# Performance work log

Measured on AMD Instinct MI355X. Metric: run time of the kernel, lower is better.

Reference implementation:

```python
import jax, jax.numpy as jnp
import numpy as np

EPS = 1e-12  # F.normalize default eps
TEMPERATURE = 0.1


def setup_inputs() -> dict:
    key = jax.random.key(0)
    ks = jax.random.split(key, 7)
    B, C, H, W = 8, 640, 64, 64
    R, KD = 4, 160           # max_refs, key_dim = context_dim // compress_ratio
    hh, ww = H // 4, W // 4  # cached value resolution from adaptive_avg_pool2d
    return {
        "current_context": jax.random.normal(ks[0], (B, C, H, W), dtype=jnp.float32),
        "Wq": jax.random.normal(ks[1], (KD, C), dtype=jnp.float32) * 0.02,  # query_proj 1x1 conv weight
        "bq": jax.random.normal(ks[2], (KD,), dtype=jnp.float32) * 0.02,
        "memory_keys": jax.random.normal(ks[3], (R, KD), dtype=jnp.float32),
        "value_cache": jax.random.normal(ks[4], (R, B, C, hh, ww), dtype=jnp.float32),
        "Wg": jax.random.normal(ks[5], (C, 2 * C), dtype=jnp.float32) * 0.02,  # fusion_gate 1x1 conv weight
        "bg": jax.random.normal(ks[6], (C,), dtype=jnp.float32) * 0.02,
        "k": 2,
    }


def reference(current_context, Wq, bq, memory_keys, value_cache, Wg, bg, k):
    B, C, H, W = current_context.shape
    R, B2, C2, hh, ww = value_cache.shape

    # query_proj (1x1 conv) then global average pool == pool then linear
    xm = current_context.mean(axis=(2, 3))                    # [B, C]
    query = xm @ Wq.T + bq                                    # [B, KD]

    # cosine similarity between query and all (fully-initialized) memory keys
    qn = query / jnp.maximum(jnp.linalg.norm(query, axis=1, keepdims=True), EPS)
    kn = memory_keys / jnp.maximum(jnp.linalg.norm(memory_keys, axis=1, keepdims=True), EPS)
    sims = qn @ kn.T                                          # [B, R]

    topv, topi = jax.lax.top_k(sims, k)                       # [B, k]
    attn = jax.nn.softmax(topv / TEMPERATURE, axis=1)         # [B, k]

    # gather cached (pooled) values per (batch, top-k index)
    gathered = value_cache[topi, jnp.arange(B)[:, None]]      # [B, k, C, hh, ww]

    # bilinear upsample (half-pixel centers == torch align_corners=False)
    resized = jax.image.resize(gathered.reshape(B * k, C, hh, ww),
                               (B * k, C, H, W), method="linear")
    resized = resized.reshape(B, k, C, H, W)

    weighted_ref = jnp.einsum("bkchw,bk->bchw", resized, attn)  # [B, C, H, W]

    # fusion gate: sigmoid(Conv1x1(cat([x, weighted_ref], dim=1))) without materializing cat
    W1, W2 = Wg[:, :C], Wg[:, C:]
    gate_pre = (jnp.einsum("bdhw,cd->bchw", current_context, W1)
                + jnp.einsum("bdhw,cd->bchw", weighted_ref, W2)
                + bg[None, :, None, None])
    gate = jax.nn.sigmoid(gate_pre)

    fused = gate * weighted_ref + (1.0 - gate) * current_context
    return fused
```

## Files before the change

kernel.cpp:

```cpp
#include <hip/hip_runtime.h>
#include <hip/hip_bf16.h>
#include <stdint.h>

#define BB 8
#define CC 640
#define HWSZ 4096
#define RR 4
#define KD 160
#define VH 16
#define VW 16
#define KW 1280
#define KX 640
#define TEMP 0.1f

#define BM 128
#define BN 64
#define BK 64

typedef __bf16 bf16x8 __attribute__((ext_vector_type(8)));
typedef short  short8 __attribute__((ext_vector_type(8)));
typedef float  f32x4  __attribute__((ext_vector_type(4)));

__device__ __forceinline__ unsigned short f2bf(float f) {
    union { float f; uint32_t u; } v; v.f = f;
    uint32_t u = v.u;
    uint32_t r = u + 0x7FFFu + ((u >> 16) & 1u);
    return (unsigned short)(r >> 16);
}
__device__ __forceinline__ float bf2f(unsigned short s) {
    union { uint32_t u; float f; } v; v.u = ((uint32_t)s) << 16;
    return v.f;
}

__global__ void k_mean(const float* __restrict__ cc, float* __restrict__ xm) {
    int plane = blockIdx.x;
    const float4* p4 = (const float4*)(cc + (size_t)plane * HWSZ);
    int t = threadIdx.x;
    float s = 0.f;
    #pragma unroll
    for (int i = 0; i < 4; i++) {
        float4 v = p4[t + i * 256];
        s += v.x + v.y + v.z + v.w;
    }
    #pragma unroll
    for (int off = 32; off; off >>= 1) s += __shfl_down(s, off);
    __shared__ float red[4];
    if ((t & 63) == 0) red[t >> 6] = s;
    __syncthreads();
    if (t == 0) xm[plane] = (red[0] + red[1] + red[2] + red[3]) * (1.f / HWSZ);
}

__global__ void k_wbf(const float* __restrict__ Wg, unsigned short* __restrict__ Wbf) {
    int i = (blockIdx.x * 256 + threadIdx.x) * 8;
    short8 o;
    #pragma unroll
    for (int j = 0; j < 8; j++) o[j] = (short)f2bf(Wg[i + j]);
    *(short8*)&Wbf[i] = o;
}

__global__ void k_query(const float* __restrict__ xm, const float* __restrict__ Wq,
                        const float* __restrict__ bq, float* __restrict__ q) {
    int o = blockIdx.x;
    int b = o / KD, j = o % KD;
    int lane = threadIdx.x;
    const float* xr = xm + b * CC;
    const float* wr = Wq + (size_t)j * CC;
    float p = 0.f;
    #pragma unroll
    for (int i = 0; i < CC / 64; i++) {
        int kk = lane + i * 64;
        p += xr[kk] * wr[kk];
    }
    #pragma unroll
    for (int off = 32; off; off >>= 1) p += __shfl_down(p, off);
    if (lane == 0) q[o] = p + bq[j];
}

__global__ void k_attn2(const float* __restrict__ q, const float* __restrict__ mk,
                        float* __restrict__ attnw, int* __restrict__ topidx) {
    int t = threadIdx.x, lane = t & 63, b = t >> 6;
    __shared__ float smk[RR * KD];
    for (int i = t; i < RR * KD; i += 512) smk[i] = mk[i];
    __syncthreads();
    const float* qr = q + b * KD;
    float qv[3];
    float s = 0.f;
    #pragma unroll
    for (int i = 0; i < 3; i++) {
        int idx = lane + i * 64;
        qv[i] = (idx < KD) ? qr[idx] : 0.f;
        s += qv[i] * qv[i];
    }
    #pragma unroll
    for (int off = 32; off; off >>= 1) s += __shfl_xor(s, off);
    float qn = fmaxf(sqrtf(s), 1e-12f);
    float sims[RR];
    #pragma unroll
    for (int r = 0; r < RR; r++) {
        float d = 0.f, kn2 = 0.f;
        #pragma unroll
        for (int i = 0; i < 3; i++) {
            int idx = lane + i * 64;
            float m = (idx < KD) ? smk[r * KD + idx] : 0.f;
            d += qv[i] * m;
            kn2 += m * m;
        }
        #pragma unroll
        for (int off = 32; off; off >>= 1) {
            d += __shfl_xor(d, off);
            kn2 += __shfl_xor(kn2, off);
        }
        sims[r] = d / (qn * fmaxf(sqrtf(kn2), 1e-12f));
    }
    if (lane == 0) {
        int i1 = 0;
        for (int r = 1; r < RR; r++) if (sims[r] > sims[i1]) i1 = r;
        int i2 = -1;
        for (int r = 0; r < RR; r++) { if (r == i1) continue; if (i2 < 0 || sims[r] > sims[i2]) i2 = r; }
        float e2 = expf((sims[i2] - sims[i1]) / TEMP);
        float a1 = 1.f / (1.f + e2);
        attnw[b * 2 + 0] = a1;
        attnw[b * 2 + 1] = e2 * a1;
        topidx[b * 2 + 0] = i1;
        topidx[b * 2 + 1] = i2;
    }
}

__global__ void k_wref(const float* __restrict__ vc, const float* __restrict__ attnw,
                       const int* __restrict__ topidx, unsigned short* __restrict__ wrb,
                       unsigned short* __restrict__ combT) {
    int blk = blockIdx.x;
    int b = blk / CC, c = blk % CC;
    __shared__ float plane[VH * VW];
    int t = threadIdx.x;
    int i1 = topidx[b * 2], i2 = topidx[b * 2 + 1];
    float a1 = attnw[b * 2], a2 = attnw[b * 2 + 1];
    const float* p1 = vc + ((size_t)(i1 * BB + b) * CC + c) * (VH * VW);
    const float* p2 = vc + ((size_t)(i2 * BB + b) * CC + c) * (VH * VW);
    plane[t] = a1 * p1[t] + a2 * p2[t];
    __syncthreads();
    combT[((size_t)((b << 8) + t)) * KX + c] = f2bf(plane[t]);
    unsigned short* out = wrb + ((size_t)b * CC + c) * HWSZ;
    #pragma unroll
    for (int i = 0; i < 16; i++) {
        int idx = t + i * 256;
        int y = idx >> 6, x = idx & 63;
        float py = y * 0.25f - 0.375f;
        int iy = (int)floorf(py);
        float fy = py - (float)iy;
        int y0 = max(iy, 0), y1 = min(iy + 1, VH - 1);
        float px = x * 0.25f - 0.375f;
        int ix = (int)floorf(px);
        float fx = px - (float)ix;
        int x0 = max(ix, 0), x1 = min(ix + 1, VW - 1);
        float v00 = plane[y0 * VW + x0], v01 = plane[y0 * VW + x1];
        float v10 = plane[y1 * VW + x0], v11 = plane[y1 * VW + x1];
        float v = (1.f - fy) * ((1.f - fx) * v00 + fx * v01)
                +        fy  * ((1.f - fx) * v10 + fx * v11);
        out[idx] = f2bf(v);
    }
}

__global__ void k_xpose(const float* __restrict__ cc, unsigned short* __restrict__ Xbf) {
    int g = blockIdx.x * 256 + threadIdx.x;
    int p = g & (HWSZ - 1);
    int idx = g >> 12;
    int kc = idx % 80;
    int b = idx / 80;
    const float* s = cc + ((size_t)(b * CC + kc * 8)) * HWSZ + p;
    short8 o;
    #pragma unroll
    for (int j = 0; j < 8; j++) o[j] = (short)f2bf(s[(size_t)j * HWSZ]);
    *(short8*)&Xbf[((size_t)b * HWSZ + p) * KX + kc * 8] = o;
}

__global__ __launch_bounds__(256) void k_gemmlow(
    const unsigned short* __restrict__ Wbf,
    const unsigned short* __restrict__ combT,
    unsigned short* __restrict__ glow)
{
    __shared__ unsigned short Wt[BM * BK];
    __shared__ unsigned short Xt[BN * BK];

    const int t = threadIdx.x;
    const int lane = t & 63;
    const int w = t >> 6;
    const int mt = blockIdx.x;
    const int n0 = blockIdx.y * BN;
    const int b = n0 >> 8;
    const int yx0 = n0 & 255;
    const int mbase = mt * BM;

    f32x4 acc[4][2];
    #pragma unroll
    for (int i = 0; i < 4; i++)
        #pragma unroll
        for (int j = 0; j < 2; j++) acc[i][j] = (f32x4){0.f, 0.f, 0.f, 0.f};

    const int wm = (w >> 1) * 64;
    const int wn = (w & 1) * 32;
    const int lrow = lane & 15;
    const int lkoff = (lane >> 4) * 8;

    const int srow = t >> 3, spos = t & 7;
    const int soct = spos ^ (srow & 7);

    const unsigned short* wsrc0 = Wbf + (size_t)mbase * KW + CC;
    const unsigned short* xsrc0 = combT + (size_t)n0 * KX;
    const int ldsbase = (t & ~63) * 8;

    for (int ks = 0; ks < KX / BK; ks++) {
        const int kb = ks * BK;
        if (ks) __syncthreads();
        #pragma unroll
        for (int i = 0; i < 4; i++) {
            const unsigned short* gw = wsrc0 + (size_t)(i * 32 + srow) * KW + kb + soct * 8;
            unsigned short* lw = &Wt[i * 2048 + ldsbase];
            __builtin_amdgcn_global_load_lds((const __attribute__((address_space(1))) void*)gw,
                                             (__attribute__((address_space(3))) void*)lw, 16, 0, 0);
        }
        #pragma unroll
        for (int i = 0; i < 2; i++) {
            const unsigned short* gx = xsrc0 + (size_t)(i * 32 + srow) * KX + kb + soct * 8;
            unsigned short* lx = &Xt[i * 2048 + ldsbase];
            __builtin_amdgcn_global_load_lds((const __attribute__((address_space(1))) void*)gx,
                                             (__attribute__((address_space(3))) void*)lx, 16, 0, 0);
        }
        __syncthreads();

        #pragma unroll
        for (int ki = 0; ki < 2; ki++) {
            bf16x8 af[4], bfr[2];
            const int kk = ki * 32 + lkoff;
            #pragma unroll
            for (int mi = 0; mi < 4; mi++) {
                int row = wm + mi * 16 + lrow;
                af[mi] = *(const bf16x8*)&Wt[row * BK + (kk ^ ((row & 7) << 3))];
            }
            #pragma unroll
            for (int ni = 0; ni < 2; ni++) {
                int prow = wn + ni * 16 + lrow;
                bfr[ni] = *(const bf16x8*)&Xt[prow * BK + (kk ^ ((prow & 7) << 3))];
            }
            #pragma unroll
            for (int mi = 0; mi < 4; mi++)
                #pragma unroll
                for (int ni = 0; ni < 2; ni++)
                    acc[mi][ni] = __builtin_amdgcn_mfma_f32_16x16x32_bf16(af[mi], bfr[ni], acc[mi][ni], 0, 0, 0);
        }
    }

    #pragma unroll
    for (int mi = 0; mi < 4; mi++) {
        #pragma unroll
        for (int r = 0; r < 4; r++) {
            int ch = mbase + wm + mi * 16 + (lane >> 4) * 4 + r;
            #pragma unroll
            for (int ni = 0; ni < 2; ni++) {
                int yx = yx0 + wn + ni * 16 + (lane & 15);
                glow[(((size_t)b * CC + ch) << 8) + yx] = f2bf(acc[mi][ni][r]);
            }
        }
    }
}

__global__ __launch_bounds__(256) void k_gemm(
    const unsigned short* __restrict__ Wbf,
    const unsigned short* __restrict__ Xbf,
    const float* __restrict__ cc,
    const unsigned short* __restrict__ wrb,
    const unsigned short* __restrict__ glow,
    const float* __restrict__ bg,
    float* __restrict__ out)
{
    __shared__ unsigned short Wt[BM * BK];
    __shared__ unsigned short Xt[BN * BK];

    const int t = threadIdx.x;
    const int lane = t & 63;
    const int w = t >> 6;

    const int orig = blockIdx.x;
    const int bid = (orig & 7) * 320 + (orig >> 3);
    const int mt = bid % 5;
    const int nt = (bid / 5) % 64;
    const int b = bid / 320;
    const int mbase = mt * BM;
    const int hwbase = nt * BN;

    f32x4 acc[4][2];
    #pragma unroll
    for (int i = 0; i < 4; i++)
        #pragma unroll
        for (int j = 0; j < 2; j++) acc[i][j] = (f32x4){0.f, 0.f, 0.f, 0.f};

    const int wm = (w >> 1) * 64;
    const int wn = (w & 1) * 32;
    const int lrow = lane & 15;
    const int lkoff = (lane >> 4) * 8;

    const int srow = t >> 3, spos = t & 7;
    const int soct = spos ^ (srow & 7);

    const unsigned short* wsrc0 = Wbf + (size_t)mbase * KW;
    const unsigned short* xsrc0 = Xbf + ((size_t)b * HWSZ + hwbase) * KX;
    const int ldsbase = (t & ~63) * 8;

    for (int ks = 0; ks < KX / BK; ks++) {
        const int kb = ks * BK;
        if (ks) __syncthreads();
        #pragma unroll
        for (int i = 0; i < 4; i++) {
            const unsigned short* gw = wsrc0 + (size_t)(i * 32 + srow) * KW + kb + soct * 8;
            unsigned short* lw = &Wt[i * 2048 + ldsbase];
            __builtin_amdgcn_global_load_lds((const __attribute__((address_space(1))) void*)gw,
                                             (__attribute__((address_space(3))) void*)lw, 16, 0, 0);
        }
        #pragma unroll
        for (int i = 0; i < 2; i++) {
            const unsigned short* gx = xsrc0 + (size_t)(i * 32 + srow) * KX + kb + soct * 8;
            unsigned short* lx = &Xt[i * 2048 + ldsbase];
            __builtin_amdgcn_global_load_lds((const __attribute__((address_space(1))) void*)gx,
                                             (__attribute__((address_space(3))) void*)lx, 16, 0, 0);
        }
        __syncthreads();

        #pragma unroll
        for (int ki = 0; ki < 2; ki++) {
            bf16x8 af[4], bfr[2];
            const int kk = ki * 32 + lkoff;
            #pragma unroll
            for (int mi = 0; mi < 4; mi++) {
                int row = wm + mi * 16 + lrow;
                af[mi] = *(const bf16x8*)&Wt[row * BK + (kk ^ ((row & 7) << 3))];
            }
            #pragma unroll
            for (int ni = 0; ni < 2; ni++) {
                int prow = wn + ni * 16 + lrow;
                bfr[ni] = *(const bf16x8*)&Xt[prow * BK + (kk ^ ((prow & 7) << 3))];
            }
            #pragma unroll
            for (int mi = 0; mi < 4; mi++)
                #pragma unroll
                for (int ni = 0; ni < 2; ni++)
                    acc[mi][ni] = __builtin_amdgcn_mfma_f32_16x16x32_bf16(af[mi], bfr[ni], acc[mi][ni], 0, 0, 0);
        }
    }

    float wq[2][4]; int qoff[2][4];
    #pragma unroll
    for (int ni = 0; ni < 2; ni++) {
        int pix = hwbase + wn + ni * 16 + (lane & 15);
        int y = pix >> 6, x = pix & 63;
        float py = y * 0.25f - 0.375f;
        int iy = (int)floorf(py);
        float fy = py - (float)iy;
        int y0 = max(iy, 0), y1 = min(iy + 1, VH - 1);
        float px = x * 0.25f - 0.375f;
        int ix = (int)floorf(px);
        float fx = px - (float)ix;
        int x0 = max(ix, 0), x1 = min(ix + 1, VW - 1);
        wq[ni][0] = (1.f - fy) * (1.f - fx);
        wq[ni][1] = (1.f - fy) * fx;
        wq[ni][2] = fy * (1.f - fx);
        wq[ni][3] = fy * fx;
        qoff[ni][0] = y0 * VW + x0;
        qoff[ni][1] = y0 * VW + x1;
        qoff[ni][2] = y1 * VW + x0;
        qoff[ni][3] = y1 * VW + x1;
    }

    const size_t pb = (size_t)b * CC * HWSZ;
    #pragma unroll
    for (int mi = 0; mi < 4; mi++) {
        #pragma unroll
        for (int r = 0; r < 4; r++) {
            int ch = mbase + wm + mi * 16 + (lane >> 4) * 4 + r;
            float bgv = bg[ch];
            size_t rowoff = pb + (size_t)ch * HWSZ;
            const unsigned short* gl = glow + (((size_t)b * CC + ch) << 8);
            #pragma unroll
            for (int ni = 0; ni < 2; ni++) {
                int pix = hwbase + wn + ni * 16 + (lane & 15);
                float gv = wq[ni][0] * bf2f(gl[qoff[ni][0]])
                         + wq[ni][1] * bf2f(gl[qoff[ni][1]])
                         + wq[ni][2] * bf2f(gl[qoff[ni][2]])
                         + wq[ni][3] * bf2f(gl[qoff[ni][3]]);
                float gp = acc[mi][ni][r] + gv + bgv;
                float g = 1.f / (1.f + expf(-gp));
                float wv = bf2f(wrb[rowoff + pix]);
                float cv = cc[rowoff + pix];
                out[rowoff + pix] = g * wv + (1.f - g) * cv;
            }
        }
    }
}

extern "C" void kernel_launch(void* const* d_in, const int* in_sizes, int n_in,
                              void* d_out, int out_size, void* d_ws, size_t ws_size,
                              hipStream_t stream) {
    const float* cc = (const float*)d_in[0];
    const float* Wq = (const float*)d_in[1];
    const float* bq = (const float*)d_in[2];
    const float* mk = (const float*)d_in[3];
    const float* vc = (const float*)d_in[4];
    const float* Wg = (const float*)d_in[5];
    const float* bg = (const float*)d_in[6];
    float* out = (float*)d_out;

    char* ws = (char*)d_ws;
    float* xm            = (float*)ws;
    float* attnw         = (float*)(ws + 20480);
    int*   topidx        = (int*)(ws + 20544);
    float* q             = (float*)(ws + 20608);
    unsigned short* Wbf  = (unsigned short*)(ws + 25728);
    unsigned short* wrb  = (unsigned short*)(ws + 1664128);
    unsigned short* Xbf  = (unsigned short*)(ws + 43607168);
    unsigned short* combT= (unsigned short*)(ws + 85550208);
    unsigned short* glow = (unsigned short*)(ws + 88171648);

    k_mean<<<BB * CC, 256, 0, stream>>>(cc, xm);
    k_wbf<<<(CC * KW) / (256 * 8), 256, 0, stream>>>(Wg, Wbf);
    k_query<<<BB * KD, 64, 0, stream>>>(xm, Wq, bq, q);
    k_attn2<<<1, 512, 0, stream>>>(q, mk, attnw, topidx);
    k_wref<<<BB * CC, 256, 0, stream>>>(vc, attnw, topidx, wrb, combT);
    k_xpose<<<(BB * 80 * HWSZ) / 256, 256, 0, stream>>>(cc, Xbf);
    dim3 gl(5, (BB * 256) / BN);
    k_gemmlow<<<gl, 256, 0, stream>>>(Wbf, combT, glow);
    k_gemm<<<2560, 256, 0, stream>>>(Wbf, Xbf, cc, wrb, glow, bg, out);
}
```

Measured before the change: 146.9 us.

## Fuse mean with transpose and upsample weighted ref inside GEMM epilogue

```diff
diff --git a/kernel.cpp b/kernel.cpp
--- a/kernel.cpp
+++ b/kernel.cpp
@@ -32,22 +32,50 @@
     return v.f;
 }
 
-__global__ void k_mean(const float* __restrict__ cc, float* __restrict__ xm) {
-    int plane = blockIdx.x;
-    const float4* p4 = (const float4*)(cc + (size_t)plane * HWSZ);
+__global__ __launch_bounds__(256) void k_xpmean(const float* __restrict__ cc,
+                                               unsigned short* __restrict__ Xbf,
+                                               float* __restrict__ part) {
+    __shared__ unsigned short T[256 * 72];
+    int blk = blockIdx.x;
+    int b = blk / 160, rr = blk % 160;
+    int ct = rr >> 4, pt = rr & 15;
+    int c0 = ct * 64, p0 = pt * 256;
     int t = threadIdx.x;
+    const float* base = cc + ((size_t)b * CC + c0) * HWSZ + p0;
+
+    {
+        int c = t >> 2, sub = t & 3;
+        const float4* row = (const float4*)(base + (size_t)c * HWSZ + sub * 64);
+        float s = 0.f;
+        #pragma unroll
+        for (int k = 0; k < 16; k++) {
+            float4 v = row[k];
+            s += v.x + v.y + v.z + v.w;
+        }
+        s += __shfl_xor(s, 1);
+        s += __shfl_xor(s, 2);
+        if (sub == 0) part[((size_t)b * CC + c0 + c) * 16 + pt] = s;
+    }
+
+    for (int c = 0; c < 64; c++) {
+        float v = base[(size_t)c * HWSZ + t];
+        T[t * 72 + (c ^ ((t & 3) << 4))] = f2bf(v);
+    }
+    __syncthreads();
+    unsigned short* dst = Xbf + ((size_t)b * HWSZ + p0 + t) * KX + c0;
+    #pragma unroll
+    for (int ch8 = 0; ch8 < 8; ch8++) {
+        short8 v = *(short8*)&T[t * 72 + ((ch8 * 8) ^ ((t & 3) << 4))];
+        *(short8*)&dst[ch8 * 8] = v;
+    }
+}
+
+__global__ void k_xmred(const float* __restrict__ part, float* __restrict__ xm) {
+    int i = blockIdx.x * 256 + threadIdx.x;
     float s = 0.f;
     #pragma unroll
-    for (int i = 0; i < 4; i++) {
-        float4 v = p4[t + i * 256];
-        s += v.x + v.y + v.z + v.w;
-    }
-    #pragma unroll
-    for (int off = 32; off; off >>= 1) s += __shfl_down(s, off);
-    __shared__ float red[4];
-    if ((t & 63) == 0) red[t >> 6] = s;
-    __syncthreads();
-    if (t == 0) xm[plane] = (red[0] + red[1] + red[2] + red[3]) * (1.f / HWSZ);
+    for (int k = 0; k < 16; k++) s += part[(size_t)i * 16 + k];
+    xm[i] = s * (1.f / HWSZ);
 }
 
 __global__ void k_wbf(const float* __restrict__ Wg, unsigned short* __restrict__ Wbf) {
@@ -126,52 +154,28 @@
     }
 }
 
-__global__ void k_wref(const float* __restrict__ vc, const float* __restrict__ attnw,
-                       const int* __restrict__ topidx, unsigned short* __restrict__ wrb,
-                       unsigned short* __restrict__ combT) {
+__global__ void k_wref8(const float* __restrict__ vc, const float* __restrict__ attnw,
+                        const int* __restrict__ topidx, unsigned short* __restrict__ comb,
+                        unsigned short* __restrict__ combT) {
     int blk = blockIdx.x;
-    int b = blk / CC, c = blk % CC;
-    __shared__ float plane[VH * VW];
+    int b = blk / 80, c8 = blk % 80;
+    int c0 = c8 * 8;
     int t = threadIdx.x;
+    __shared__ unsigned short S[256 * 8];
     int i1 = topidx[b * 2], i2 = topidx[b * 2 + 1];
     float a1 = attnw[b * 2], a2 = attnw[b * 2 + 1];
-    const float* p1 = vc + ((size_t)(i1 * BB + b) * CC + c) * (VH * VW);
-    const float* p2 = vc + ((size_t)(i2 * BB + b) * CC + c) * (VH * VW);
-    plane[t] = a1 * p1[t] + a2 * p2[t];
+    const float* p1 = vc + ((size_t)(i1 * BB + b) * CC + c0) * 256;
+    const float* p2 = vc + ((size_t)(i2 * BB + b) * CC + c0) * 256;
+    #pragma unroll
+    for (int j = 0; j < 8; j++) {
+        float v = a1 * p1[j * 256 + t] + a2 * p2[j * 256 + t];
+        unsigned short us = f2bf(v);
+        comb[((size_t)b * CC + c0 + j) * 256 + t] = us;
+        S[t * 8 + j] = us;
+    }
     __syncthreads();
-    combT[((size_t)((b << 8) + t)) * KX + c] = f2bf(plane[t]);
-    unsigned short* out = wrb + ((size_t)b * CC + c) * HWSZ;
-    #pragma unroll
-    for (int i = 0; i < 16; i++) {
-        int idx = t + i * 256;
-        int y = idx >> 6, x = idx & 63;
-        float py = y * 0.25f - 0.375f;
-        int iy = (int)floorf(py);
-        float fy = py - (float)iy;
-        int y0 = max(iy, 0), y1 = min(iy + 1, VH - 1);
-        float px = x * 0.25f - 0.375f;
-        int ix = (int)floorf(px);
-        float fx = px - (float)ix;
-        int x0 = max(ix, 0), x1 = min(ix + 1, VW - 1);
-        float v00 = plane[y0 * VW + x0], v01 = plane[y0 * VW + x1];
-        float v10 = plane[y1 * VW + x0], v11 = plane[y1 * VW + x1];
-        float v = (1.f - fy) * ((1.f - fx) * v00 + fx * v01)
-                +        fy  * ((1.f - fx) * v10 + fx * v11);
-        out[idx] = f2bf(v);
-    }
-}
-
-__global__ void k_xpose(const float* __restrict__ cc, unsigned short* __restrict__ Xbf) {
-    int g = blockIdx.x * 256 + threadIdx.x;
-    int p = g & (HWSZ - 1);
-    int idx = g >> 12;
-    int kc = idx % 80;
-    int b = idx / 80;
-    const float* s = cc + ((size_t)(b * CC + kc * 8)) * HWSZ + p;
-    short8 o;
-    #pragma unroll
-    for (int j = 0; j < 8; j++) o[j] = (short)f2bf(s[(size_t)j * HWSZ]);
-    *(short8*)&Xbf[((size_t)b * HWSZ + p) * KX + kc * 8] = o;
+    short8 o = *(short8*)&S[t * 8];
+    *(short8*)&combT[((size_t)((b << 8) + t)) * KX + c0] = o;
 }
 
 __global__ __launch_bounds__(256) void k_gemmlow(
@@ -268,13 +272,14 @@
     const unsigned short* __restrict__ Wbf,
     const unsigned short* __restrict__ Xbf,
     const float* __restrict__ cc,
-    const unsigned short* __restrict__ wrb,
+    const unsigned short* __restrict__ comb,
     const unsigned short* __restrict__ glow,
     const float* __restrict__ bg,
     float* __restrict__ out)
 {
-    __shared__ unsigned short Wt[BM * BK];
-    __shared__ unsigned short Xt[BN * BK];
+    __shared__ unsigned short SM[BM * BK + BN * BK];
+    unsigned short* Wt = SM;
+    unsigned short* Xt = SM + BM * BK;
 
     const int t = threadIdx.x;
     const int lane = t & 63;
@@ -347,27 +352,40 @@
         }
     }
 
-    float wq[2][4]; int qoff[2][4];
-    #pragma unroll
-    for (int ni = 0; ni < 2; ni++) {
-        int pix = hwbase + wn + ni * 16 + (lane & 15);
-        int y = pix >> 6, x = pix & 63;
-        float py = y * 0.25f - 0.375f;
+    __syncthreads();
+    float* gy = (float*)SM;
+    float* cy = gy + 128 * 17;
+    {
+        float py = nt * 0.25f - 0.375f;
         int iy = (int)floorf(py);
         float fy = py - (float)iy;
         int y0 = max(iy, 0), y1 = min(iy + 1, VH - 1);
-        float px = x * 0.25f - 0.375f;
-        int ix = (int)floorf(px);
-        float fx = px - (float)ix;
-        int x0 = max(ix, 0), x1 = min(ix + 1, VW - 1);
-        wq[ni][0] = (1.f - fy) * (1.f - fx);
-        wq[ni][1] = (1.f - fy) * fx;
-        wq[ni][2] = fy * (1.f - fx);
-        wq[ni][3] = fy * fx;
-        qoff[ni][0] = y0 * VW + x0;
-        qoff[ni][1] = y0 * VW + x1;
-        qoff[ni][2] = y1 * VW + x0;
-        qoff[ni][3] = y1 * VW + x1;
+        const unsigned short* gb = glow + (((size_t)b * CC + mbase) << 8);
+        const unsigned short* cb = comb + (((size_t)b * CC + mbase) << 8);
+        #pragma unroll
+        for (int i = 0; i < 8; i++) {
+            int e = t + i * 256;
+            int chl = e >> 4, x16 = e & 15;
+            size_t base = ((size_t)chl << 8);
+            float g0 = bf2f(gb[base + y0 * 16 + x16]);
+            float g1 = bf2f(gb[base + y1 * 16 + x16]);
+            gy[chl * 17 + x16] = g0 + fy * (g1 - g0);
+            float c0v = bf2f(cb[base + y0 * 16 + x16]);
+            float c1v = bf2f(cb[base + y1 * 16 + x16]);
+            cy[chl * 17 + x16] = c0v + fy * (c1v - c0v);
+        }
+    }
+    __syncthreads();
+
+    float fxv[2]; int x0i[2], x1i[2];
+    #pragma unroll
+    for (int ni = 0; ni < 2; ni++) {
+        int x = wn + ni * 16 + lrow;
+        float pxx = x * 0.25f - 0.375f;
+        int ix = (int)floorf(pxx);
+        fxv[ni] = pxx - (float)ix;
+        x0i[ni] = max(ix, 0);
+        x1i[ni] = min(ix + 1, VW - 1);
     }
 
     const size_t pb = (size_t)b * CC * HWSZ;
@@ -375,20 +393,21 @@
     for (int mi = 0; mi < 4; mi++) {
         #pragma unroll
         for (int r = 0; r < 4; r++) {
-            int ch = mbase + wm + mi * 16 + (lane >> 4) * 4 + r;
+            int chl = wm + mi * 16 + (lane >> 4) * 4 + r;
+            int ch = mbase + chl;
             float bgv = bg[ch];
             size_t rowoff = pb + (size_t)ch * HWSZ;
-            const unsigned short* gl = glow + (((size_t)b * CC + ch) << 8);
             #pragma unroll
             for (int ni = 0; ni < 2; ni++) {
-                int pix = hwbase + wn + ni * 16 + (lane & 15);
-                float gv = wq[ni][0] * bf2f(gl[qoff[ni][0]])
-                         + wq[ni][1] * bf2f(gl[qoff[ni][1]])
-                         + wq[ni][2] * bf2f(gl[qoff[ni][2]])
-                         + wq[ni][3] * bf2f(gl[qoff[ni][3]]);
+                int pix = hwbase + wn + ni * 16 + lrow;
+                float g0 = gy[chl * 17 + x0i[ni]];
+                float g1 = gy[chl * 17 + x1i[ni]];
+                float gv = g0 + fxv[ni] * (g1 - g0);
+                float w0 = cy[chl * 17 + x0i[ni]];
+                float w1 = cy[chl * 17 + x1i[ni]];
+                float wv = w0 + fxv[ni] * (w1 - w0);
                 float gp = acc[mi][ni][r] + gv + bgv;
                 float g = 1.f / (1.f + expf(-gp));
-                float wv = bf2f(wrb[rowoff + pix]);
                 float cv = cc[rowoff + pix];
                 out[rowoff + pix] = g * wv + (1.f - g) * cv;
             }
@@ -409,23 +428,24 @@
     float* out = (float*)d_out;
 
     char* ws = (char*)d_ws;
-    float* xm            = (float*)ws;
-    float* attnw         = (float*)(ws + 20480);
-    int*   topidx        = (int*)(ws + 20544);
-    float* q             = (float*)(ws + 20608);
-    unsigned short* Wbf  = (unsigned short*)(ws + 25728);
-    unsigned short* wrb  = (unsigned short*)(ws + 1664128);
-    unsigned short* Xbf  = (unsigned short*)(ws + 43607168);
-    unsigned short* combT= (unsigned short*)(ws + 85550208);
-    unsigned short* glow = (unsigned short*)(ws + 88171648);
-
-    k_mean<<<BB * CC, 256, 0, stream>>>(cc, xm);
+    float* xm             = (float*)ws;
+    float* attnw          = (float*)(ws + 20480);
+    int*   topidx         = (int*)(ws + 20544);
+    float* q              = (float*)(ws + 20608);
+    float* part           = (float*)(ws + 25728);
+    unsigned short* Wbf   = (unsigned short*)(ws + 353408);
+    unsigned short* Xbf   = (unsigned short*)(ws + 1991808);
+    unsigned short* comb  = (unsigned short*)(ws + 43934848);
+    unsigned short* combT = (unsigned short*)(ws + 46556288);
+    unsigned short* glow  = (unsigned short*)(ws + 49177728);
+
+    k_xpmean<<<BB * 160, 256, 0, stream>>>(cc, Xbf, part);
+    k_xmred<<<20, 256, 0, stream>>>(part, xm);
     k_wbf<<<(CC * KW) / (256 * 8), 256, 0, stream>>>(Wg, Wbf);
     k_query<<<BB * KD, 64, 0, stream>>>(xm, Wq, bq, q);
     k_attn2<<<1, 512, 0, stream>>>(q, mk, attnw, topidx);
-    k_wref<<<BB * CC, 256, 0, stream>>>(vc, attnw, topidx, wrb, combT);
-    k_xpose<<<(BB * 80 * HWSZ) / 256, 256, 0, stream>>>(cc, Xbf);
+    k_wref8<<<BB * 80, 256, 0, stream>>>(vc, attnw, topidx, comb, combT);
     dim3 gl(5, (BB * 256) / BN);
     k_gemmlow<<<gl, 256, 0, stream>>>(Wbf, combT, glow);
-    k_gemm<<<2560, 256, 0, stream>>>(Wbf, Xbf, cc, wrb, glow, bg, out);
-}
+    k_gemm<<<2560, 256, 0, stream>>>(Wbf, Xbf, cc, comb, glow, bg, out);
+}
```

Result: faster. 136.6 us (-7.0%).
